# Kernel tuning notes

Measured on AMD Instinct MI355X. Metric: run time of the kernel, lower is better.

Reference implementation:

```python
import jax, jax.numpy as jnp
import numpy as np

N_NODES = 50000
N_EDGES = 800000
IN_CH = 128
HID_CH = 128


def glorot(key, shape):
    fan_in, fan_out = shape[0], shape[1]
    lim = np.sqrt(6.0 / (fan_in + fan_out)).astype(np.float32)
    return jax.random.uniform(key, shape, jnp.float32, -lim, lim)


def setup_inputs() -> dict:
    key = jax.random.key(0)
    k1, k2, k3, k4 = jax.random.split(key, 4)
    x = jax.random.normal(k1, (N_NODES, IN_CH), jnp.float32)
    edge_index = jax.random.randint(k2, (2, N_EDGES), 0, N_NODES, jnp.int64)
    W1 = glorot(k3, (IN_CH, HID_CH))
    b1 = jnp.zeros((HID_CH,), jnp.float32)
    W2 = glorot(k4, (HID_CH, HID_CH))
    b2 = jnp.zeros((HID_CH,), jnp.float32)
    return {"x": x, "edge_index": edge_index, "W1": W1, "b1": b1, "W2": W2, "b2": b2}


def _gcn_conv(x, W, b, src, dst, n_nodes):
    # PyG GCNConv: h = D^{-1/2} (A + I) D^{-1/2} (x W) + b
    h = x @ W  # [N, H] transform first (as in PyG)
    loops = jnp.arange(n_nodes, dtype=src.dtype)
    s = jnp.concatenate([src, loops])  # add self-loops
    d = jnp.concatenate([dst, loops])
    deg = jnp.zeros((n_nodes,), h.dtype).at[d].add(1.0)
    dinv = jnp.where(deg > 0, jax.lax.rsqrt(deg), 0.0)
    coef = dinv[s] * dinv[d]  # [E+N]
    msg = h[s] * coef[:, None]  # gather + scale
    out = jax.ops.segment_sum(msg, d, num_segments=n_nodes)  # scatter-add
    return out + b


def reference(x, edge_index, W1, b1, W2, b2):
    src, dst = edge_index[0], edge_index[1]
    n = x.shape[0]
    h = jax.nn.relu(_gcn_conv(x, W1, b1, src, dst, n))
    h = jax.nn.relu(_gcn_conv(h, W2, b2, src, dst, n))
    return h
```

## Files before the change

kernel.cpp:

```cpp
#include <hip/hip_runtime.h>

#define N_NODES 50000
#define N_EDGES 800000
#define CH 128
#define NBUCK 196
#define B_BIN 250
#define CHUNK 3200
#define G_GEMM 782

typedef __attribute__((ext_vector_type(8))) short bf16x8;
typedef __attribute__((ext_vector_type(8))) unsigned short u16x8;
typedef __attribute__((ext_vector_type(4))) float f32x4;

__device__ __forceinline__ float bf2f(unsigned short u) {
    union { unsigned int i; float f; } c;
    c.i = ((unsigned int)u) << 16;
    return c.f;
}
__device__ __forceinline__ unsigned short f2bf(float f) {
    union { float f; unsigned int i; } c;
    c.f = f;
    unsigned int lsb = (c.i >> 16) & 1u;
    c.i += 0x7fffu + lsb;
    return (unsigned short)(c.i >> 16);
}

__global__ __launch_bounds__(256) void k_wt(const float* __restrict__ Wa,
                                            const float* __restrict__ Wb,
                                            unsigned short* __restrict__ Wta,
                                            unsigned short* __restrict__ Wtb) {
    const float* W = blockIdx.x ? Wb : Wa;
    unsigned short* Wt = blockIdx.x ? Wtb : Wta;
    const int tid = threadIdx.x;
    for (int i = 0; i < 64; ++i) {
        int idx = i * 256 + tid;
        int n = idx >> 7, kk = idx & 127;
        Wt[idx] = f2bf(W[kk * CH + n]);
    }
}

__global__ __launch_bounds__(256) void k_mega(
        const int* __restrict__ ei, int* __restrict__ blk_base,
        const float* __restrict__ X, const unsigned short* __restrict__ Wt1,
        unsigned short* __restrict__ HS1u) {
    const int tid = threadIdx.x;
    const int b = blockIdx.x;

    if (b < B_BIN) {
        __shared__ int h[NBUCK];
        for (int i = tid; i < NBUCK; i += 256) h[i] = 0;
        __syncthreads();
        const int e0 = b * CHUNK;
        const int* dst = ei + N_EDGES;
        for (int i = tid; i < CHUNK; i += 256)
            atomicAdd(&h[dst[e0 + i] >> 8], 1);
        __syncthreads();
        for (int k = tid; k < NBUCK; k += 256)
            blk_base[b * NBUCK + k] = h[k];
        return;
    }

    const int gb = b - B_BIN;
    const int l = tid & 63, w = tid >> 6;
    const int lm = l & 15, lk = l >> 4;
    const int row0 = gb * 64 + w * 16;

    int arow = row0 + lm;
    if (arow >= N_NODES) arow = N_NODES - 1;
    bf16x8 a[4];
    #pragma unroll
    for (int ki = 0; ki < 4; ++ki) {
        const float* ap = &X[arow * CH + ki * 32 + lk * 8];
        float4 f0 = *(const float4*)ap;
        float4 f1 = *(const float4*)(ap + 4);
        bf16x8 af;
        af[0] = (short)f2bf(f0.x); af[1] = (short)f2bf(f0.y);
        af[2] = (short)f2bf(f0.z); af[3] = (short)f2bf(f0.w);
        af[4] = (short)f2bf(f1.x); af[5] = (short)f2bf(f1.y);
        af[6] = (short)f2bf(f1.z); af[7] = (short)f2bf(f1.w);
        a[ki] = af;
    }

    #pragma unroll
    for (int ct = 0; ct < 8; ++ct) {
        const unsigned short* wp = &Wt1[(ct * 16 + lm) * CH + lk * 8];
        f32x4 acc = {0.f, 0.f, 0.f, 0.f};
        #pragma unroll
        for (int ki = 0; ki < 4; ++ki) {
            bf16x8 bfrag = *(const bf16x8*)&wp[ki * 32];
            acc = __builtin_amdgcn_mfma_f32_16x16x32_bf16(a[ki], bfrag, acc, 0, 0, 0);
        }
        #pragma unroll
        for (int r = 0; r < 4; ++r) {
            int row = row0 + lk * 4 + r;
            if (row < N_NODES)
                HS1u[row * CH + ct * 16 + lm] = f2bf(acc[r]);
        }
    }
}

__global__ __launch_bounds__(256) void k_colscan(int* __restrict__ blk_base,
                                                 int* __restrict__ bucket_cnt) {
    __shared__ int sm[256];
    const int tid = threadIdx.x, k = blockIdx.x;
    int v = (tid < B_BIN) ? blk_base[tid * NBUCK + k] : 0;
    sm[tid] = v;
    __syncthreads();
    #pragma unroll
    for (int off = 1; off < 256; off <<= 1) {
        int t = (tid >= off) ? sm[tid - off] : 0;
        __syncthreads();
        sm[tid] += t;
        __syncthreads();
    }
    if (tid < B_BIN) blk_base[tid * NBUCK + k] = sm[tid] - v;
    if (tid == 255) bucket_cnt[k] = sm[255];
}

__global__ __launch_bounds__(256) void k_bin_place(const int* __restrict__ ei,
                                                   const int* __restrict__ bucket_cnt,
                                                   const int* __restrict__ blk_base,
                                                   unsigned int* __restrict__ ebuf) {
    __shared__ int sm[256];
    __shared__ int bbase[NBUCK];
    __shared__ int h[NBUCK];
    const int tid = threadIdx.x, b = blockIdx.x;

    int v = (tid < NBUCK) ? bucket_cnt[tid] : 0;
    sm[tid] = v;
    __syncthreads();
    #pragma unroll
    for (int off = 1; off < 256; off <<= 1) {
        int t = (tid >= off) ? sm[tid - off] : 0;
        __syncthreads();
        sm[tid] += t;
        __syncthreads();
    }
    if (tid < NBUCK) bbase[tid] = sm[tid] - v;
    for (int i = tid; i < NBUCK; i += 256) h[i] = 0;
    __syncthreads();

    const int e0 = b * CHUNK;
    for (int i = tid; i < CHUNK; i += 256) {
        int s = ei[e0 + i];
        int d = ei[N_EDGES + e0 + i];
        int k = d >> 8;
        int loc = atomicAdd(&h[k], 1);
        int pos = bbase[k] + blk_base[b * NBUCK + k] + loc;
        ebuf[pos] = ((unsigned int)s << 8) | (unsigned int)(d & 255);
    }
}

__global__ __launch_bounds__(256) void k_bucket_csr(const unsigned int* __restrict__ ebuf,
                                                    const int* __restrict__ bucket_cnt,
                                                    int* __restrict__ rowptr,
                                                    int* __restrict__ col,
                                                    float* __restrict__ dinv,
                                                    unsigned short* __restrict__ HS1u) {
    __shared__ int cnts[256];
    __shared__ int fillc[256];
    __shared__ int sm[256];
    __shared__ float sdinv[256];
    __shared__ int e0s;
    const int tid = threadIdx.x, k = blockIdx.x;
    const int node0 = k << 8;

    int vb = (tid < NBUCK) ? bucket_cnt[tid] : 0;
    sm[tid] = vb;
    __syncthreads();
    #pragma unroll
    for (int off = 1; off < 256; off <<= 1) {
        int t = (tid >= off) ? sm[tid - off] : 0;
        __syncthreads();
        sm[tid] += t;
        __syncthreads();
    }
    if (tid == k) e0s = sm[tid] - vb;
    cnts[tid] = 0;
    __syncthreads();
    const int e0 = e0s;
    const int cnt = bucket_cnt[k];

    for (int i = tid; i < cnt; i += 256)
        atomicAdd(&cnts[ebuf[e0 + i] & 255], 1);
    __syncthreads();

    int v = cnts[tid];
    sm[tid] = v;
    __syncthreads();
    #pragma unroll
    for (int off = 1; off < 256; off <<= 1) {
        int t = (tid >= off) ? sm[tid - off] : 0;
        __syncthreads();
        sm[tid] += t;
        __syncthreads();
    }
    int rp = sm[tid] - v;
    fillc[tid] = rp;
    float dval = rsqrtf((float)(v + 1));
    sdinv[tid] = dval;
    int node = node0 + tid;
    if (node < N_NODES) {
        rowptr[node] = e0 + rp;
        dinv[node] = dval;
    }
    if (k == NBUCK - 1 && tid == 0) rowptr[N_NODES] = N_EDGES;
    __syncthreads();

    for (int i = tid; i < cnt; i += 256) {
        unsigned int pv = ebuf[e0 + i];
        int j = pv & 255;
        int loc = atomicAdd(&fillc[j], 1);
        col[e0 + loc] = (int)(pv >> 8);
    }

    ushort4* H4 = (ushort4*)HS1u;
    #pragma unroll 4
    for (int t = 0; t < 32; ++t) {
        int u = t * 256 + tid;
        int r = u >> 5, c = u & 31;
        int nd = node0 + r;
        if (nd < N_NODES) {
            ushort4 v4 = H4[nd * 32 + c];
            float sc = sdinv[r];
            v4.x = f2bf(bf2f(v4.x) * sc);
            v4.y = f2bf(bf2f(v4.y) * sc);
            v4.z = f2bf(bf2f(v4.z) * sc);
            v4.w = f2bf(bf2f(v4.w) * sc);
            H4[nd * 32 + c] = v4;
        }
    }
}

template <int MODE>
__global__ __launch_bounds__(256) void k_agg(
        const int* __restrict__ rowptr, const int* __restrict__ col,
        const unsigned short* __restrict__ H, const float* __restrict__ dinv,
        const float* __restrict__ b, unsigned short* __restrict__ OUT) {
    int gid = blockIdx.x * 256 + threadIdx.x;
    int node = gid >> 4;
    if (node >= N_NODES) return;
    int lane = gid & 15;
    const u16x8* H8 = (const u16x8*)H;

    int e0 = rowptr[node];
    int e1 = rowptr[node + 1];

    u16x8 hv = H8[node * 16 + lane];
    float acc[8];
    #pragma unroll
    for (int j = 0; j < 8; ++j) acc[j] = bf2f(hv[j]);

    int e = e0;
    for (; e + 3 < e1; e += 4) {
        int s0 = col[e], s1 = col[e + 1], s2 = col[e + 2], s3 = col[e + 3];
        u16x8 v0 = H8[s0 * 16 + lane];
        u16x8 v1 = H8[s1 * 16 + lane];
        u16x8 v2 = H8[s2 * 16 + lane];
        u16x8 v3 = H8[s3 * 16 + lane];
        #pragma unroll
        for (int j = 0; j < 8; ++j)
            acc[j] += (bf2f(v0[j]) + bf2f(v1[j])) + (bf2f(v2[j]) + bf2f(v3[j]));
    }
    for (; e < e1; ++e) {
        u16x8 v = H8[col[e] * 16 + lane];
        #pragma unroll
        for (int j = 0; j < 8; ++j) acc[j] += bf2f(v[j]);
    }

    float di = dinv[node];
    u16x8 o;
    if (MODE == 0) {
        float4 b0 = *(const float4*)&b[lane * 8];
        float4 b1v = *(const float4*)&b[lane * 8 + 4];
        float bb[8] = {b0.x, b0.y, b0.z, b0.w, b1v.x, b1v.y, b1v.z, b1v.w};
        #pragma unroll
        for (int j = 0; j < 8; ++j)
            o[j] = f2bf(fmaxf(acc[j] * di + bb[j], 0.f) * di);
    } else {
        #pragma unroll
        for (int j = 0; j < 8; ++j)
            o[j] = f2bf(acc[j] * di);
    }
    *(u16x8*)&OUT[node * CH + lane * 8] = o;
}

__global__ __launch_bounds__(256) void k_gemm_out(
        const unsigned short* __restrict__ A2,
        const unsigned short* __restrict__ Wt2,
        const float* __restrict__ b2,
        float* __restrict__ OUT) {
    const int tid = threadIdx.x;
    const int l = tid & 63, w = tid >> 6;
    const int lm = l & 15, lk = l >> 4;
    const int row0 = blockIdx.x * 64 + w * 16;

    int arow = row0 + lm;
    if (arow >= N_NODES) arow = N_NODES - 1;
    bf16x8 a[4];
    #pragma unroll
    for (int ki = 0; ki < 4; ++ki)
        a[ki] = *(const bf16x8*)&A2[arow * CH + ki * 32 + lk * 8];

    #pragma unroll
    for (int ct = 0; ct < 8; ++ct) {
        const unsigned short* wp = &Wt2[(ct * 16 + lm) * CH + lk * 8];
        f32x4 acc = {0.f, 0.f, 0.f, 0.f};
        #pragma unroll
        for (int ki = 0; ki < 4; ++ki) {
            bf16x8 bfrag = *(const bf16x8*)&wp[ki * 32];
            acc = __builtin_amdgcn_mfma_f32_16x16x32_bf16(a[ki], bfrag, acc, 0, 0, 0);
        }
        float bb = b2[ct * 16 + lm];
        #pragma unroll
        for (int r = 0; r < 4; ++r) {
            int row = row0 + lk * 4 + r;
            if (row < N_NODES)
                OUT[row * CH + ct * 16 + lm] = fmaxf(acc[r] + bb, 0.f);
        }
    }
}

extern "C" void kernel_launch(void* const* d_in, const int* in_sizes, int n_in,
                              void* d_out, int out_size, void* d_ws, size_t ws_size,
                              hipStream_t stream) {
    const float* x  = (const float*)d_in[0];
    const int*   ei = (const int*)d_in[1];
    const float* W1 = (const float*)d_in[2];
    const float* b1 = (const float*)d_in[3];
    const float* W2 = (const float*)d_in[4];
    const float* b2 = (const float*)d_in[5];
    float* out = (float*)d_out;

    int* blk_base    = (int*)d_ws;
    int* bucket_cnt  = blk_base + 49152;
    int* rowptr      = bucket_cnt + 256;
    int* col         = rowptr + 50176;
    float* dinv      = (float*)(col + 800256);
    unsigned int* ebuf = (unsigned int*)(dinv + 50176);
    unsigned short* hs1 = (unsigned short*)(ebuf + 800256);
    unsigned short* h1p = hs1 + 6400000;
    unsigned short* a2  = h1p + 6400000;
    unsigned short* wt1 = a2 + 6400000;
    unsigned short* wt2 = wt1 + 16384;

    const int gAgg = 3125;

    k_wt<<<2, 256, 0, stream>>>(W1, W2, wt1, wt2);
    k_mega<<<B_BIN + G_GEMM, 256, 0, stream>>>(ei, blk_base, x, wt1, hs1);
    k_colscan<<<NBUCK, 256, 0, stream>>>(blk_base, bucket_cnt);
    k_bin_place<<<B_BIN, 256, 0, stream>>>(ei, bucket_cnt, blk_base, ebuf);
    k_bucket_csr<<<NBUCK, 256, 0, stream>>>(ebuf, bucket_cnt, rowptr, col, dinv, hs1);
    k_agg<0><<<gAgg, 256, 0, stream>>>(rowptr, col, hs1, dinv, b1, h1p);
    k_agg<1><<<gAgg, 256, 0, stream>>>(rowptr, col, h1p, dinv, nullptr, a2);
    k_gemm_out<<<G_GEMM, 256, 0, stream>>>(a2, wt2, b2, out);
}
```

Baseline: 152.6 us.

## Fuse CSR build into cooperative kernel and fold source degree scaling into aggregation

```diff
diff --git a/kernel.cpp b/kernel.cpp
--- a/kernel.cpp
+++ b/kernel.cpp
@@ -1,4 +1,7 @@
 #include <hip/hip_runtime.h>
+#include <hip/hip_cooperative_groups.h>
+
+namespace cg = cooperative_groups;
 
 #define N_NODES 50000
 #define N_EDGES 800000
@@ -99,135 +102,119 @@
     }
 }
 
-__global__ __launch_bounds__(256) void k_colscan(int* __restrict__ blk_base,
-                                                 int* __restrict__ bucket_cnt) {
+__global__ __launch_bounds__(256) void k_csr_coop(
+        const int* __restrict__ ei, int* __restrict__ blk_base,
+        int* __restrict__ bucket_cnt, unsigned int* __restrict__ ebuf,
+        int* __restrict__ rowptr, int* __restrict__ degc,
+        int* __restrict__ col) {
+    cg::grid_group grid = cg::this_grid();
     __shared__ int sm[256];
-    const int tid = threadIdx.x, k = blockIdx.x;
-    int v = (tid < B_BIN) ? blk_base[tid * NBUCK + k] : 0;
-    sm[tid] = v;
-    __syncthreads();
-    #pragma unroll
-    for (int off = 1; off < 256; off <<= 1) {
-        int t = (tid >= off) ? sm[tid - off] : 0;
-        __syncthreads();
-        sm[tid] += t;
-        __syncthreads();
-    }
-    if (tid < B_BIN) blk_base[tid * NBUCK + k] = sm[tid] - v;
-    if (tid == 255) bucket_cnt[k] = sm[255];
-}
-
-__global__ __launch_bounds__(256) void k_bin_place(const int* __restrict__ ei,
-                                                   const int* __restrict__ bucket_cnt,
-                                                   const int* __restrict__ blk_base,
-                                                   unsigned int* __restrict__ ebuf) {
-    __shared__ int sm[256];
-    __shared__ int bbase[NBUCK];
-    __shared__ int h[NBUCK];
-    const int tid = threadIdx.x, b = blockIdx.x;
-
-    int v = (tid < NBUCK) ? bucket_cnt[tid] : 0;
-    sm[tid] = v;
-    __syncthreads();
-    #pragma unroll
-    for (int off = 1; off < 256; off <<= 1) {
-        int t = (tid >= off) ? sm[tid - off] : 0;
-        __syncthreads();
-        sm[tid] += t;
-        __syncthreads();
-    }
-    if (tid < NBUCK) bbase[tid] = sm[tid] - v;
-    for (int i = tid; i < NBUCK; i += 256) h[i] = 0;
-    __syncthreads();
-
-    const int e0 = b * CHUNK;
-    for (int i = tid; i < CHUNK; i += 256) {
-        int s = ei[e0 + i];
-        int d = ei[N_EDGES + e0 + i];
-        int k = d >> 8;
-        int loc = atomicAdd(&h[k], 1);
-        int pos = bbase[k] + blk_base[b * NBUCK + k] + loc;
-        ebuf[pos] = ((unsigned int)s << 8) | (unsigned int)(d & 255);
-    }
-}
-
-__global__ __launch_bounds__(256) void k_bucket_csr(const unsigned int* __restrict__ ebuf,
-                                                    const int* __restrict__ bucket_cnt,
-                                                    int* __restrict__ rowptr,
-                                                    int* __restrict__ col,
-                                                    float* __restrict__ dinv,
-                                                    unsigned short* __restrict__ HS1u) {
-    __shared__ int cnts[256];
+    __shared__ int aux[NBUCK];
+    __shared__ int h[256];
     __shared__ int fillc[256];
-    __shared__ int sm[256];
-    __shared__ float sdinv[256];
     __shared__ int e0s;
-    const int tid = threadIdx.x, k = blockIdx.x;
-    const int node0 = k << 8;
-
-    int vb = (tid < NBUCK) ? bucket_cnt[tid] : 0;
-    sm[tid] = vb;
-    __syncthreads();
-    #pragma unroll
-    for (int off = 1; off < 256; off <<= 1) {
-        int t = (tid >= off) ? sm[tid - off] : 0;
-        __syncthreads();
-        sm[tid] += t;
-        __syncthreads();
-    }
-    if (tid == k) e0s = sm[tid] - vb;
-    cnts[tid] = 0;
-    __syncthreads();
-    const int e0 = e0s;
-    const int cnt = bucket_cnt[k];
-
-    for (int i = tid; i < cnt; i += 256)
-        atomicAdd(&cnts[ebuf[e0 + i] & 255], 1);
-    __syncthreads();
-
-    int v = cnts[tid];
-    sm[tid] = v;
-    __syncthreads();
-    #pragma unroll
-    for (int off = 1; off < 256; off <<= 1) {
-        int t = (tid >= off) ? sm[tid - off] : 0;
-        __syncthreads();
-        sm[tid] += t;
-        __syncthreads();
-    }
-    int rp = sm[tid] - v;
-    fillc[tid] = rp;
-    float dval = rsqrtf((float)(v + 1));
-    sdinv[tid] = dval;
-    int node = node0 + tid;
-    if (node < N_NODES) {
-        rowptr[node] = e0 + rp;
-        dinv[node] = dval;
-    }
-    if (k == NBUCK - 1 && tid == 0) rowptr[N_NODES] = N_EDGES;
-    __syncthreads();
-
-    for (int i = tid; i < cnt; i += 256) {
-        unsigned int pv = ebuf[e0 + i];
-        int j = pv & 255;
-        int loc = atomicAdd(&fillc[j], 1);
-        col[e0 + loc] = (int)(pv >> 8);
-    }
-
-    ushort4* H4 = (ushort4*)HS1u;
-    #pragma unroll 4
-    for (int t = 0; t < 32; ++t) {
-        int u = t * 256 + tid;
-        int r = u >> 5, c = u & 31;
-        int nd = node0 + r;
-        if (nd < N_NODES) {
-            ushort4 v4 = H4[nd * 32 + c];
-            float sc = sdinv[r];
-            v4.x = f2bf(bf2f(v4.x) * sc);
-            v4.y = f2bf(bf2f(v4.y) * sc);
-            v4.z = f2bf(bf2f(v4.z) * sc);
-            v4.w = f2bf(bf2f(v4.w) * sc);
-            H4[nd * 32 + c] = v4;
+    const int tid = threadIdx.x;
+    const int b = blockIdx.x;
+
+    if (b < NBUCK) {
+        const int k = b;
+        int v = (tid < B_BIN) ? blk_base[tid * NBUCK + k] : 0;
+        sm[tid] = v;
+        __syncthreads();
+        #pragma unroll
+        for (int off = 1; off < 256; off <<= 1) {
+            int t = (tid >= off) ? sm[tid - off] : 0;
+            __syncthreads();
+            sm[tid] += t;
+            __syncthreads();
+        }
+        if (tid < B_BIN) blk_base[tid * NBUCK + k] = sm[tid] - v;
+        if (tid == 255) bucket_cnt[k] = sm[255];
+    }
+    __threadfence();
+    grid.sync();
+
+    if (b < B_BIN) {
+        int v = (tid < NBUCK) ? bucket_cnt[tid] : 0;
+        sm[tid] = v;
+        __syncthreads();
+        #pragma unroll
+        for (int off = 1; off < 256; off <<= 1) {
+            int t = (tid >= off) ? sm[tid - off] : 0;
+            __syncthreads();
+            sm[tid] += t;
+            __syncthreads();
+        }
+        if (tid < NBUCK) aux[tid] = sm[tid] - v;
+        for (int i = tid; i < NBUCK; i += 256) h[i] = 0;
+        __syncthreads();
+
+        const int e0 = b * CHUNK;
+        for (int i = tid; i < CHUNK; i += 256) {
+            int s = ei[e0 + i];
+            int d = ei[N_EDGES + e0 + i];
+            int k = d >> 8;
+            int loc = atomicAdd(&h[k], 1);
+            int pos = aux[k] + blk_base[b * NBUCK + k] + loc;
+            ebuf[pos] = ((unsigned int)s << 8) | (unsigned int)(d & 255);
+        }
+    }
+    __threadfence();
+    grid.sync();
+
+    int e0v = 0, cntv = 0;
+    if (b < NBUCK) {
+        const int k = b;
+        int vb = (tid < NBUCK) ? bucket_cnt[tid] : 0;
+        sm[tid] = vb;
+        __syncthreads();
+        #pragma unroll
+        for (int off = 1; off < 256; off <<= 1) {
+            int t = (tid >= off) ? sm[tid - off] : 0;
+            __syncthreads();
+            sm[tid] += t;
+            __syncthreads();
+        }
+        if (tid == k) e0s = sm[tid] - vb;
+        h[tid] = 0;
+        __syncthreads();
+        e0v = e0s;
+        cntv = bucket_cnt[k];
+
+        for (int i = tid; i < cntv; i += 256)
+            atomicAdd(&h[ebuf[e0v + i] & 255], 1);
+        __syncthreads();
+
+        int v = h[tid];
+        sm[tid] = v;
+        __syncthreads();
+        #pragma unroll
+        for (int off = 1; off < 256; off <<= 1) {
+            int t = (tid >= off) ? sm[tid - off] : 0;
+            __syncthreads();
+            sm[tid] += t;
+            __syncthreads();
+        }
+        int rp = sm[tid] - v;
+        fillc[tid] = rp;
+        int node = (k << 8) + tid;
+        if (node < N_NODES) {
+            rowptr[node] = e0v + rp;
+            int dc = v + 1;
+            degc[node] = dc > 255 ? 255 : dc;
+        }
+        if (k == NBUCK - 1 && tid == 0) rowptr[N_NODES] = N_EDGES;
+    }
+    __threadfence();
+    grid.sync();
+
+    if (b < NBUCK) {
+        for (int i = tid; i < cntv; i += 256) {
+            unsigned int pv = ebuf[e0v + i];
+            int s = (int)(pv >> 8);
+            int j = pv & 255;
+            int loc = atomicAdd(&fillc[j], 1);
+            col[e0v + loc] = (s << 8) | degc[s];
         }
     }
 }
@@ -235,7 +222,7 @@
 template <int MODE>
 __global__ __launch_bounds__(256) void k_agg(
         const int* __restrict__ rowptr, const int* __restrict__ col,
-        const unsigned short* __restrict__ H, const float* __restrict__ dinv,
+        const unsigned short* __restrict__ H,
         const float* __restrict__ b, unsigned short* __restrict__ OUT) {
     int gid = blockIdx.x * 256 + threadIdx.x;
     int node = gid >> 4;
@@ -245,30 +232,49 @@
 
     int e0 = rowptr[node];
     int e1 = rowptr[node + 1];
+    float di = rsqrtf((float)(e1 - e0 + 1));
 
     u16x8 hv = H8[node * 16 + lane];
     float acc[8];
     #pragma unroll
-    for (int j = 0; j < 8; ++j) acc[j] = bf2f(hv[j]);
+    for (int j = 0; j < 8; ++j)
+        acc[j] = MODE == 0 ? bf2f(hv[j]) * di : bf2f(hv[j]);
 
     int e = e0;
     for (; e + 3 < e1; e += 4) {
-        int s0 = col[e], s1 = col[e + 1], s2 = col[e + 2], s3 = col[e + 3];
-        u16x8 v0 = H8[s0 * 16 + lane];
-        u16x8 v1 = H8[s1 * 16 + lane];
-        u16x8 v2 = H8[s2 * 16 + lane];
-        u16x8 v3 = H8[s3 * 16 + lane];
-        #pragma unroll
-        for (int j = 0; j < 8; ++j)
-            acc[j] += (bf2f(v0[j]) + bf2f(v1[j])) + (bf2f(v2[j]) + bf2f(v3[j]));
+        int c0 = col[e], c1 = col[e + 1], c2 = col[e + 2], c3 = col[e + 3];
+        u16x8 v0 = H8[(c0 >> 8) * 16 + lane];
+        u16x8 v1 = H8[(c1 >> 8) * 16 + lane];
+        u16x8 v2 = H8[(c2 >> 8) * 16 + lane];
+        u16x8 v3 = H8[(c3 >> 8) * 16 + lane];
+        if (MODE == 0) {
+            float d0 = rsqrtf((float)(c0 & 255));
+            float d1 = rsqrtf((float)(c1 & 255));
+            float d2 = rsqrtf((float)(c2 & 255));
+            float d3 = rsqrtf((float)(c3 & 255));
+            #pragma unroll
+            for (int j = 0; j < 8; ++j)
+                acc[j] += (bf2f(v0[j]) * d0 + bf2f(v1[j]) * d1)
+                        + (bf2f(v2[j]) * d2 + bf2f(v3[j]) * d3);
+        } else {
+            #pragma unroll
+            for (int j = 0; j < 8; ++j)
+                acc[j] += (bf2f(v0[j]) + bf2f(v1[j])) + (bf2f(v2[j]) + bf2f(v3[j]));
+        }
     }
     for (; e < e1; ++e) {
-        u16x8 v = H8[col[e] * 16 + lane];
-        #pragma unroll
-        for (int j = 0; j < 8; ++j) acc[j] += bf2f(v[j]);
-    }
-
-    float di = dinv[node];
+        int c0 = col[e];
+        u16x8 v = H8[(c0 >> 8) * 16 + lane];
+        if (MODE == 0) {
+            float ds = rsqrtf((float)(c0 & 255));
+            #pragma unroll
+            for (int j = 0; j < 8; ++j) acc[j] += bf2f(v[j]) * ds;
+        } else {
+            #pragma unroll
+            for (int j = 0; j < 8; ++j) acc[j] += bf2f(v[j]);
+        }
+    }
+
     u16x8 o;
     if (MODE == 0) {
         float4 b0 = *(const float4*)&b[lane * 8];
@@ -335,11 +341,11 @@
     int* blk_base    = (int*)d_ws;
     int* bucket_cnt  = blk_base + 49152;
     int* rowptr      = bucket_cnt + 256;
-    int* col         = rowptr + 50176;
-    float* dinv      = (float*)(col + 800256);
-    unsigned int* ebuf = (unsigned int*)(dinv + 50176);
-    unsigned short* hs1 = (unsigned short*)(ebuf + 800256);
-    unsigned short* h1p = hs1 + 6400000;
+    int* degc        = rowptr + 50176;
+    int* col         = degc + 50176;
+    unsigned int* ebuf = (unsigned int*)(col + 800256);
+    unsigned short* hs1u = (unsigned short*)(ebuf + 800256);
+    unsigned short* h1p = hs1u + 6400000;
     unsigned short* a2  = h1p + 6400000;
     unsigned short* wt1 = a2 + 6400000;
     unsigned short* wt2 = wt1 + 16384;
@@ -347,11 +353,17 @@
     const int gAgg = 3125;
 
     k_wt<<<2, 256, 0, stream>>>(W1, W2, wt1, wt2);
-    k_mega<<<B_BIN + G_GEMM, 256, 0, stream>>>(ei, blk_base, x, wt1, hs1);
-    k_colscan<<<NBUCK, 256, 0, stream>>>(blk_base, bucket_cnt);
-    k_bin_place<<<B_BIN, 256, 0, stream>>>(ei, bucket_cnt, blk_base, ebuf);
-    k_bucket_csr<<<NBUCK, 256, 0, stream>>>(ebuf, bucket_cnt, rowptr, col, dinv, hs1);
-    k_agg<0><<<gAgg, 256, 0, stream>>>(rowptr, col, hs1, dinv, b1, h1p);
-    k_agg<1><<<gAgg, 256, 0, stream>>>(rowptr, col, h1p, dinv, nullptr, a2);
+    k_mega<<<B_BIN + G_GEMM, 256, 0, stream>>>(ei, blk_base, x, wt1, hs1u);
+
+    {
+        const int* ei_ = ei;
+        void* args[] = {(void*)&ei_, (void*)&blk_base, (void*)&bucket_cnt,
+                        (void*)&ebuf, (void*)&rowptr, (void*)&degc, (void*)&col};
+        hipLaunchCooperativeKernel((const void*)k_csr_coop, dim3(256), dim3(256),
+                                   args, 0, stream);
+    }
+
+    k_agg<0><<<gAgg, 256, 0, stream>>>(rowptr, col, hs1u, b1, h1p);
+    k_agg<1><<<gAgg, 256, 0, stream>>>(rowptr, col, h1p, nullptr, a2);
     k_gemm_out<<<G_GEMM, 256, 0, stream>>>(a2, wt2, b2, out);
 }
```

Result: slower. 324.3 us (+112.5%).
